# Kernel optimization log

Measured on AMD Instinct MI355X. Metric: run time of the kernel, lower is better.

The kernel has to match this reference:

```python
import jax, jax.numpy as jnp
import numpy as np

BATCH = 128
N_BLOCKS = 14        # num_channel_blocks (num_ofdm_symbols)
T = 1096             # num_time_samples (fft_size + cp_length)
L_TOT = 24           # channel impulse response length


def _toeplitz_g(num_time_samples, l_tot):
    # Reproduces scipy.linalg.toeplitz(first_col, first_row):
    #   g[i, j] = first_col[i - j] if i >= j else first_row[j - i]
    first_col = np.concatenate([np.arange(num_time_samples), np.full(l_tot - 1, num_time_samples)])
    first_row = np.concatenate([[0], np.full(l_tot - 1, num_time_samples)])
    d = np.arange(num_time_samples + l_tot - 1)[:, None] - np.arange(l_tot)[None, :]
    g = np.where(d >= 0, first_col[np.maximum(d, 0)], first_row[np.maximum(-d, 0)])
    return g.astype(np.int32)  # [T + l_tot - 1, l_tot]

_G = jnp.asarray(_toeplitz_g(T, L_TOT))


def setup_inputs() -> dict:
    key = jax.random.key(0)
    kx, kh = jax.random.split(key)
    x = jax.random.normal(kx, (BATCH, N_BLOCKS, T), dtype=jnp.float32)
    h_time = jax.random.normal(kh, (BATCH, N_BLOCKS, L_TOT), dtype=jnp.float32)
    return {"x": x, "h_time": h_time}


def reference(x, h_time):
    # Pad so index T maps to zero (out-of-range taps)
    x_pad = jnp.pad(x, ((0, 0), (0, 0), (0, 1)))          # [B, N, T+1]
    xg = x_pad[..., _G]                                    # [B, N, T+L_TOT-1, L_TOT]
    y = jnp.einsum('bntl,bnl->bnt', xg, h_time)            # batched matvec
    # overlap_and_add with frame_step = T
    frame_len = T + L_TOT - 1
    out_len = (N_BLOCKS - 1) * T + frame_len
    pos = jnp.asarray(np.arange(frame_len)[None, :] + np.arange(N_BLOCKS)[:, None] * T)  # [N, frame_len]
    out = jnp.zeros((x.shape[0], out_len), y.dtype).at[:, pos].add(y)
    return out
```

## Files before the change

kernel.cpp:

```cpp
#include <hip/hip_runtime.h>

#define BATCH  128
#define NB     14
#define TS     1096
#define LTOT   24
#define FRAME  (TS + LTOT - 1)
#define OUTLEN ((NB - 1) * TS + FRAME)
#define XLEN   (NB * TS)
#define BS     256

__global__ __launch_bounds__(256)
void atc_lds_kernel(const float* __restrict__ x,
                    const float* __restrict__ h,
                    float* __restrict__ out) {
    const int b   = blockIdx.y;
    const int o0  = blockIdx.x * BS;
    const int tid = threadIdx.x;
    const int o   = o0 + tid;

    __shared__ __align__(16) float xs[BS + 32];
    const float* __restrict__ xb = x + (size_t)b * XLEN;

    if (tid < 72) {
        const int g = o0 - 32 + 4 * tid;
        const float* gp = xb + g;
        float4 v;
        if (g >= 0 && g + 4 <= XLEN) {
            v = *(const float4*)gp;
        } else {
            v.x = ((unsigned)(g + 0) < (unsigned)XLEN) ? gp[0] : 0.f;
            v.y = ((unsigned)(g + 1) < (unsigned)XLEN) ? gp[1] : 0.f;
            v.z = ((unsigned)(g + 2) < (unsigned)XLEN) ? gp[2] : 0.f;
            v.w = ((unsigned)(g + 3) < (unsigned)XLEN) ? gp[3] : 0.f;
        }
        *(float4*)(&xs[4 * tid]) = v;
    }
    __syncthreads();

    int pa = o0 - 23;      if (pa < 0) pa = 0;
    int pb = o0 + BS - 1;  if (pb > XLEN - 1) pb = XLEN - 1;
    const int fa = pa / TS;
    const int fb = pb / TS;

    const float* __restrict__ hA = h + ((size_t)b * NB + fa) * LTOT;
    float hwA[LTOT];
    #pragma unroll
    for (int q = 0; q < 6; ++q) {
        float4 v = *(const float4*)(hA + 4 * q);
        hwA[4*q] = v.x; hwA[4*q+1] = v.y; hwA[4*q+2] = v.z; hwA[4*q+3] = v.w;
    }

    float acc = 0.f;
    if (fa == fb) {
        #pragma unroll
        for (int j = 0; j < LTOT; ++j)
            acc = fmaf(hwA[j], xs[32 + tid - j], acc);
    } else {
        const float* __restrict__ hB = h + ((size_t)b * NB + fb) * LTOT;
        float hwB[LTOT];
        #pragma unroll
        for (int q = 0; q < 6; ++q) {
            float4 v = *(const float4*)(hB + 4 * q);
            hwB[4*q] = v.x; hwB[4*q+1] = v.y; hwB[4*q+2] = v.z; hwB[4*q+3] = v.w;
        }
        const int sB = fb * TS;
        #pragma unroll
        for (int j = 0; j < LTOT; ++j) {
            const float hv = (o - j >= sB) ? hwB[j] : hwA[j];
            acc = fmaf(hv, xs[32 + tid - j], acc);
        }
    }

    if (o < OUTLEN)
        out[(size_t)b * OUTLEN + o] = acc;
}

extern "C" void kernel_launch(void* const* d_in, const int* in_sizes, int n_in,
                              void* d_out, int out_size, void* d_ws, size_t ws_size,
                              hipStream_t stream) {
    const float* x = (const float*)d_in[0];
    const float* h = (const float*)d_in[1];
    float* out = (float*)d_out;

    dim3 block(BS, 1, 1);
    dim3 grid((OUTLEN + BS - 1) / BS, BATCH, 1);
    atc_lds_kernel<<<grid, block, 0, stream>>>(x, h, out);
}
```

Measured before the change: 11.91 us.

## Compute four outputs per thread with register-cached input window

Each thread now produces four consecutive outputs. It loads a 28-element window of x from LDS into registers with float4 reads, so every LDS value is reused across four outputs instead of being read once per tap per output. The block tile grows to 1024 outputs, which cuts the number of blocks and the redundant halo loads and h-row loads. The costs are higher register pressure, fewer blocks for a small problem (about 15x128 blocks), and a three-way branch for tiles that straddle a frame boundary.

Result: slower. 13.39 us (+12.4%).

```diff
diff --git a/kernel.cpp b/kernel.cpp
--- a/kernel.cpp
+++ b/kernel.cpp
@@ -8,71 +8,114 @@
 #define OUTLEN ((NB - 1) * TS + FRAME)
 #define XLEN   (NB * TS)
 #define BS     256
+#define OPT    4
+#define TILE   (BS * OPT)
 
 __global__ __launch_bounds__(256)
-void atc_lds_kernel(const float* __restrict__ x,
-                    const float* __restrict__ h,
-                    float* __restrict__ out) {
+void atc_lds4_kernel(const float* __restrict__ x,
+                     const float* __restrict__ h,
+                     float* __restrict__ out) {
     const int b   = blockIdx.y;
-    const int o0  = blockIdx.x * BS;
+    const int o0  = blockIdx.x * TILE;
     const int tid = threadIdx.x;
-    const int o   = o0 + tid;
 
-    __shared__ __align__(16) float xs[BS + 32];
+    __shared__ __align__(16) float xs[TILE + 32];
     const float* __restrict__ xb = x + (size_t)b * XLEN;
 
-    if (tid < 72) {
-        const int g = o0 - 32 + 4 * tid;
-        const float* gp = xb + g;
-        float4 v;
-        if (g >= 0 && g + 4 <= XLEN) {
-            v = *(const float4*)gp;
-        } else {
-            v.x = ((unsigned)(g + 0) < (unsigned)XLEN) ? gp[0] : 0.f;
-            v.y = ((unsigned)(g + 1) < (unsigned)XLEN) ? gp[1] : 0.f;
-            v.z = ((unsigned)(g + 2) < (unsigned)XLEN) ? gp[2] : 0.f;
-            v.w = ((unsigned)(g + 3) < (unsigned)XLEN) ? gp[3] : 0.f;
+    #pragma unroll
+    for (int it = 0; it < 2; ++it) {
+        const int idx = tid + it * BS;
+        if (idx < (TILE + 32) / 4) {
+            const int g = o0 - 32 + 4 * idx;
+            float4 v;
+            if (g >= 0 && g + 4 <= XLEN) {
+                v = *(const float4*)(xb + g);
+            } else {
+                v.x = ((unsigned)(g+0) < (unsigned)XLEN) ? xb[g+0] : 0.f;
+                v.y = ((unsigned)(g+1) < (unsigned)XLEN) ? xb[g+1] : 0.f;
+                v.z = ((unsigned)(g+2) < (unsigned)XLEN) ? xb[g+2] : 0.f;
+                v.w = ((unsigned)(g+3) < (unsigned)XLEN) ? xb[g+3] : 0.f;
+            }
+            *(float4*)(&xs[4 * idx]) = v;
         }
-        *(float4*)(&xs[4 * tid]) = v;
     }
     __syncthreads();
 
-    int pa = o0 - 23;      if (pa < 0) pa = 0;
-    int pb = o0 + BS - 1;  if (pb > XLEN - 1) pb = XLEN - 1;
+    int pa = o0 - 23;        if (pa < 0) pa = 0;
+    int pb = o0 + TILE - 1;  if (pb > XLEN - 1) pb = XLEN - 1;
     const int fa = pa / TS;
     const int fb = pb / TS;
 
-    const float* __restrict__ hA = h + ((size_t)b * NB + fa) * LTOT;
     float hwA[LTOT];
-    #pragma unroll
-    for (int q = 0; q < 6; ++q) {
-        float4 v = *(const float4*)(hA + 4 * q);
-        hwA[4*q] = v.x; hwA[4*q+1] = v.y; hwA[4*q+2] = v.z; hwA[4*q+3] = v.w;
+    {
+        const float* hr = h + ((size_t)b * NB + fa) * LTOT;
+        #pragma unroll
+        for (int q = 0; q < 6; ++q) {
+            float4 v = *(const float4*)(hr + 4 * q);
+            hwA[4*q] = v.x; hwA[4*q+1] = v.y; hwA[4*q+2] = v.z; hwA[4*q+3] = v.w;
+        }
     }
 
-    float acc = 0.f;
+    float xw[28];
+    {
+        const int base = 4 * tid + 8;
+        #pragma unroll
+        for (int q = 0; q < 7; ++q) {
+            float4 v = *(const float4*)(&xs[base + 4 * q]);
+            xw[4*q] = v.x; xw[4*q+1] = v.y; xw[4*q+2] = v.z; xw[4*q+3] = v.w;
+        }
+    }
+
+    const int o_t = o0 + 4 * tid;
+    float acc[OPT] = {0.f, 0.f, 0.f, 0.f};
+
     if (fa == fb) {
         #pragma unroll
         for (int j = 0; j < LTOT; ++j)
-            acc = fmaf(hwA[j], xs[32 + tid - j], acc);
+            #pragma unroll
+            for (int k = 0; k < OPT; ++k)
+                acc[k] = fmaf(hwA[j], xw[24 + k - j], acc[k]);
     } else {
-        const float* __restrict__ hB = h + ((size_t)b * NB + fb) * LTOT;
         float hwB[LTOT];
-        #pragma unroll
-        for (int q = 0; q < 6; ++q) {
-            float4 v = *(const float4*)(hB + 4 * q);
-            hwB[4*q] = v.x; hwB[4*q+1] = v.y; hwB[4*q+2] = v.z; hwB[4*q+3] = v.w;
+        {
+            const float* hr = h + ((size_t)b * NB + fb) * LTOT;
+            #pragma unroll
+            for (int q = 0; q < 6; ++q) {
+                float4 v = *(const float4*)(hr + 4 * q);
+                hwB[4*q] = v.x; hwB[4*q+1] = v.y; hwB[4*q+2] = v.z; hwB[4*q+3] = v.w;
+            }
         }
         const int sB = fb * TS;
-        #pragma unroll
-        for (int j = 0; j < LTOT; ++j) {
-            const float hv = (o - j >= sB) ? hwB[j] : hwA[j];
-            acc = fmaf(hv, xs[32 + tid - j], acc);
+        if (o_t - 23 >= sB || o_t + OPT - 1 < sB) {
+            const bool useB = (o_t - 23 >= sB);
+            float hw[LTOT];
+            #pragma unroll
+            for (int j = 0; j < LTOT; ++j) hw[j] = useB ? hwB[j] : hwA[j];
+            #pragma unroll
+            for (int j = 0; j < LTOT; ++j)
+                #pragma unroll
+                for (int k = 0; k < OPT; ++k)
+                    acc[k] = fmaf(hw[j], xw[24 + k - j], acc[k]);
+        } else {
+            #pragma unroll
+            for (int j = 0; j < LTOT; ++j)
+                #pragma unroll
+                for (int k = 0; k < OPT; ++k) {
+                    const float hv = (o_t + k - j >= sB) ? hwB[j] : hwA[j];
+                    acc[k] = fmaf(hv, xw[24 + k - j], acc[k]);
+                }
         }
     }
 
-    if (o < OUTLEN)
-        out[(size_t)b * OUTLEN + o] = acc;
+    float* ob = out + (size_t)b * OUTLEN + o_t;
+    if (o_t + OPT - 1 < OUTLEN) {
+        #pragma unroll
+        for (int k = 0; k < OPT; ++k) ob[k] = acc[k];
+    } else {
+        #pragma unroll
+        for (int k = 0; k < OPT; ++k)
+            if (o_t + k < OUTLEN) ob[k] = acc[k];
+    }
 }
 
 extern "C" void kernel_launch(void* const* d_in, const int* in_sizes, int n_in,
@@ -83,6 +126,6 @@
     float* out = (float*)d_out;
 
     dim3 block(BS, 1, 1);
-    dim3 grid((OUTLEN + BS - 1) / BS, BATCH, 1);
-    atc_lds_kernel<<<grid, block, 0, stream>>>(x, h, out);
+    dim3 grid((OUTLEN + TILE - 1) / TILE, BATCH, 1);
+    atc_lds4_kernel<<<grid, block, 0, stream>>>(x, h, out);
 }
```

## Use persistent blocks with double-buffered async global-to-LDS tile prefetch

Applied to the files above, without the earlier changes.

The grid shrinks to 11 blocks per batch row, and each block walks up to six consecutive 256-sample output tiles. While the current tile is being convolved, the next tile's input is prefetched into a second LDS buffer. Interior tiles use global_load_lds direct-to-LDS transfers, and edge tiles keep the guarded register path. The goal is to cut block launch and scheduling overhead and to hide load latency behind the FMA loop. In exchange the kernel runs far fewer blocks, so there is less parallelism to hide latency, and it relies on the barrier waiting for the async LDS loads to finish.

Result: slower. 13.32 us (+11.8%).

```diff
diff --git a/kernel.cpp b/kernel.cpp
--- a/kernel.cpp
+++ b/kernel.cpp
@@ -4,75 +4,114 @@
 #define NB     14
 #define TS     1096
 #define LTOT   24
-#define FRAME  (TS + LTOT - 1)
-#define OUTLEN ((NB - 1) * TS + FRAME)
+#define OUTLEN 15367
 #define XLEN   (NB * TS)
 #define BS     256
+#define TILE   256
+#define NBI    ((OUTLEN + TILE - 1) / TILE)
+#define NBX    11
+#define CHUNK  6
 
-__global__ __launch_bounds__(256)
-void atc_lds_kernel(const float* __restrict__ x,
-                    const float* __restrict__ h,
-                    float* __restrict__ out) {
+__device__ __forceinline__ void dma16(const float* g, float* l) {
+    __builtin_amdgcn_global_load_lds(
+        (const __attribute__((address_space(1))) uint32_t*)g,
+        (__attribute__((address_space(3))) uint32_t*)l, 16, 0, 0);
+}
+__device__ __forceinline__ void dma4(const float* g, float* l) {
+    __builtin_amdgcn_global_load_lds(
+        (const __attribute__((address_space(1))) uint32_t*)g,
+        (__attribute__((address_space(3))) uint32_t*)l, 4, 0, 0);
+}
+
+__global__ __launch_bounds__(BS)
+void atc_persist(const float* __restrict__ x,
+                 const float* __restrict__ h,
+                 float* __restrict__ out) {
     const int b   = blockIdx.y;
-    const int o0  = blockIdx.x * BS;
+    const int bx  = blockIdx.x;
     const int tid = threadIdx.x;
-    const int o   = o0 + tid;
 
-    __shared__ __align__(16) float xs[BS + 32];
     const float* __restrict__ xb = x + (size_t)b * XLEN;
+    const float* __restrict__ hb = h + (size_t)b * NB * LTOT;
+    float* __restrict__ ob = out + (size_t)b * OUTLEN;
 
-    if (tid < 72) {
-        const int g = o0 - 32 + 4 * tid;
-        const float* gp = xb + g;
-        float4 v;
-        if (g >= 0 && g + 4 <= XLEN) {
-            v = *(const float4*)gp;
+    __shared__ __align__(16) float xs[2][TILE + 32];
+
+    const int bi0 = bx * CHUNK;
+    const int biN = (bi0 + CHUNK < NBI) ? bi0 + CHUNK : NBI;
+
+    auto stage = [&](int bi, int c) {
+        const int g0 = bi * TILE - 32;
+        if (bi >= 1 && bi <= 58) {
+            if (tid < 64)      dma16(xb + g0 + 32 + 4 * tid, &xs[c][32 + 4 * tid]);
+            else if (tid < 96) dma4 (xb + g0 + (tid - 64),   &xs[c][tid - 64]);
         } else {
-            v.x = ((unsigned)(g + 0) < (unsigned)XLEN) ? gp[0] : 0.f;
-            v.y = ((unsigned)(g + 1) < (unsigned)XLEN) ? gp[1] : 0.f;
-            v.z = ((unsigned)(g + 2) < (unsigned)XLEN) ? gp[2] : 0.f;
-            v.w = ((unsigned)(g + 3) < (unsigned)XLEN) ? gp[3] : 0.f;
+            if (tid < 72) {
+                const int g = g0 + 4 * tid;
+                float4 v;
+                if (g >= 0 && g + 4 <= XLEN) {
+                    v = *(const float4*)(xb + g);
+                } else {
+                    v.x = ((unsigned)(g+0) < (unsigned)XLEN) ? xb[g+0] : 0.f;
+                    v.y = ((unsigned)(g+1) < (unsigned)XLEN) ? xb[g+1] : 0.f;
+                    v.z = ((unsigned)(g+2) < (unsigned)XLEN) ? xb[g+2] : 0.f;
+                    v.w = ((unsigned)(g+3) < (unsigned)XLEN) ? xb[g+3] : 0.f;
+                }
+                *(float4*)(&xs[c][4 * tid]) = v;
+            }
         }
-        *(float4*)(&xs[4 * tid]) = v;
+    };
+
+    stage(bi0, 0);
+
+    int c = 0;
+    for (int bi = bi0; bi < biN; ++bi, c ^= 1) {
+        __syncthreads();
+        if (bi + 1 < biN) stage(bi + 1, c ^ 1);
+
+        const int o0 = bi * TILE;
+        const int o  = o0 + tid;
+
+        int pa = o0 - 23;        if (pa < 0) pa = 0;
+        int pb = o0 + TILE - 1;  if (pb > XLEN - 1) pb = XLEN - 1;
+        const int fa = pa / TS;
+        const int fb = pb / TS;
+
+        float hwA[LTOT];
+        {
+            const float* hr = hb + fa * LTOT;
+            #pragma unroll
+            for (int q = 0; q < 6; ++q) {
+                float4 v = *(const float4*)(hr + 4 * q);
+                hwA[4*q]=v.x; hwA[4*q+1]=v.y; hwA[4*q+2]=v.z; hwA[4*q+3]=v.w;
+            }
+        }
+
+        float acc = 0.f;
+        if (fa == fb) {
+            #pragma unroll
+            for (int j = 0; j < LTOT; ++j)
+                acc = fmaf(hwA[j], xs[c][32 + tid - j], acc);
+        } else {
+            float hwB[LTOT];
+            {
+                const float* hr = hb + fb * LTOT;
+                #pragma unroll
+                for (int q = 0; q < 6; ++q) {
+                    float4 v = *(const float4*)(hr + 4 * q);
+                    hwB[4*q]=v.x; hwB[4*q+1]=v.y; hwB[4*q+2]=v.z; hwB[4*q+3]=v.w;
+                }
+            }
+            const int sB = fb * TS;
+            #pragma unroll
+            for (int j = 0; j < LTOT; ++j) {
+                const float hv = (o - j >= sB) ? hwB[j] : hwA[j];
+                acc = fmaf(hv, xs[c][32 + tid - j], acc);
+            }
+        }
+
+        if (o < OUTLEN) ob[o] = acc;
     }
-    __syncthreads();
-
-    int pa = o0 - 23;      if (pa < 0) pa = 0;
-    int pb = o0 + BS - 1;  if (pb > XLEN - 1) pb = XLEN - 1;
-    const int fa = pa / TS;
-    const int fb = pb / TS;
-
-    const float* __restrict__ hA = h + ((size_t)b * NB + fa) * LTOT;
-    float hwA[LTOT];
-    #pragma unroll
-    for (int q = 0; q < 6; ++q) {
-        float4 v = *(const float4*)(hA + 4 * q);
-        hwA[4*q] = v.x; hwA[4*q+1] = v.y; hwA[4*q+2] = v.z; hwA[4*q+3] = v.w;
-    }
-
-    float acc = 0.f;
-    if (fa == fb) {
-        #pragma unroll
-        for (int j = 0; j < LTOT; ++j)
-            acc = fmaf(hwA[j], xs[32 + tid - j], acc);
-    } else {
-        const float* __restrict__ hB = h + ((size_t)b * NB + fb) * LTOT;
-        float hwB[LTOT];
-        #pragma unroll
-        for (int q = 0; q < 6; ++q) {
-            float4 v = *(const float4*)(hB + 4 * q);
-            hwB[4*q] = v.x; hwB[4*q+1] = v.y; hwB[4*q+2] = v.z; hwB[4*q+3] = v.w;
-        }
-        const int sB = fb * TS;
-        #pragma unroll
-        for (int j = 0; j < LTOT; ++j) {
-            const float hv = (o - j >= sB) ? hwB[j] : hwA[j];
-            acc = fmaf(hv, xs[32 + tid - j], acc);
-        }
-    }
-
-    if (o < OUTLEN)
-        out[(size_t)b * OUTLEN + o] = acc;
 }
 
 extern "C" void kernel_launch(void* const* d_in, const int* in_sizes, int n_in,
@@ -83,6 +122,6 @@
     float* out = (float*)d_out;
 
     dim3 block(BS, 1, 1);
-    dim3 grid((OUTLEN + BS - 1) / BS, BATCH, 1);
-    atc_lds_kernel<<<grid, block, 0, stream>>>(x, h, out);
+    dim3 grid(NBX, BATCH, 1);
+    atc_persist<<<grid, block, 0, stream>>>(x, h, out);
 }
```
